# Performance work log

Hardware: AMD Instinct MI355X
Metric: run time of the kernel (lower is better)

## Reference

```python
import jax, jax.numpy as jnp
import numpy as np


def setup_inputs() -> dict:
    key = jax.random.key(0)
    k1, k2 = jax.random.split(key)
    N, K, D = 32768, 1024, 512
    x = jax.random.normal(k1, (N, D), dtype=jnp.float32)
    centers = jax.random.normal(k2, (K, D), dtype=jnp.float32)
    return {"x": x, "centers": centers}


def reference(x, centers):
    # broadcasted (x[:,None]-c[None])**2 sum without the O(N*K*D) intermediate)
    x_sq = jnp.sum(x * x, axis=-1, keepdims=True)           # [N, 1]
    c_sq = jnp.sum(centers * centers, axis=-1)              # [K]
    cross = jnp.einsum('nd,kd->nk', x, centers)             # [N, K]
    norm_squared = x_sq + c_sq[None, :] - 2.0 * cross       # [N, K]
    # exp(-d/2) / sum_k exp(-d/2) == softmax(-d/2) over clusters
    probabilities = jax.nn.softmax(-0.5 * norm_squared, axis=1)
    return probabilities
```

## Files before the change

### kernel.cpp

```cpp
#include <hip/hip_runtime.h>
#include <stdint.h>


namespace {
constexpr int N_ROWS  = 32768;
constexpr int K_CL    = 1024;
constexpr int D_DIM   = 512;
constexpr int BM      = 32;
constexpr int THREADS = 256;
constexpr int NSLICE  = 16;
}

typedef _Float16 f16_t;
typedef _Float16 f16x8 __attribute__((ext_vector_type(8)));
typedef _Float16 f16x4 __attribute__((ext_vector_type(4)));
typedef float    f32x16 __attribute__((ext_vector_type(16)));
typedef float    f32x4v __attribute__((ext_vector_type(4)));

__global__ __launch_bounds__(64) void prep_kernel(const float* __restrict__ centers,
                                                  f16_t* __restrict__ bpack,
                                                  float* __restrict__ bias) {
  const int col = blockIdx.x, lane = threadIdx.x;
  const int t  = lane >> 2;
  const int ks = (lane >> 1) & 1;
  const int kh = lane & 1;
  const float* src = centers + (size_t)col * D_DIM + lane * 8;
  f16x8 hi;
  float ssq = 0.f;
  #pragma unroll
  for (int i = 0; i < 8; ++i) {
    float v = src[i];
    ssq += v * v;
    hi[i] = (f16_t)v;
  }
  const int jh = col >> 9, cb = (col & 511) >> 5, c32 = col & 31;
  const size_t off = ((size_t)ks * 16 + cb) * 512 + (c32 * 2 + kh) * 8;
  *(f16x8*)(bpack + (size_t)(2 * t + jh) * 16384 + off) = hi;
  for (int o = 32; o; o >>= 1) ssq += __shfl_down(ssq, o, 64);
  if (lane == 0) bias[col] = -0.5f * ssq;
}

__global__ __launch_bounds__(THREADS, 2) void cluster_kernel(
    const float* __restrict__ x, const f16_t* __restrict__ bpack,
    const float* __restrict__ bias, float* __restrict__ out) {
  __shared__ __align__(16) char Ax[32768];
  __shared__ float red[4 * BM];
  __shared__ float fin[BM];

  const int tid  = threadIdx.x;
  const int w    = tid >> 6;
  const int lane = tid & 63;
  const int l31  = lane & 31;
  const int h    = lane >> 5;
  const int brow = blockIdx.x * BM;

  const char* bbase = (const char*)bpack + (w >> 1) * 32768 + (w & 1) * 8192 +
                      (l31 * 2 + h) * 16;

#define LOADB(T, KS, DST)                                                      \
  {                                                                            \
    const char* p_ = bbase + (size_t)(T) * 65536 + (KS) * 16384;               \
    _Pragma("unroll")                                                          \
    for (int cb_ = 0; cb_ < 8; ++cb_)                                          \
      (DST)[cb_] = *(const f16x8*)(p_ + cb_ * 1024);                           \
  }

  f16x8 b0[8], b1[8];
  LOADB(0, 0, b0)

  {
    const float* xsrc = x + (size_t)brow * D_DIM;
    #pragma unroll
    for (int it = 0; it < 16; ++it) {
      const int idx = it * 256 + tid;
      const int r = idx >> 7, f = idx & 127;
      f32x4v v = __builtin_nontemporal_load(
          (const f32x4v*)(xsrc + (size_t)r * D_DIM + f * 4));
      f16x4 h4;
      h4[0] = (f16_t)v[0]; h4[1] = (f16_t)v[1];
      h4[2] = (f16_t)v[2]; h4[3] = (f16_t)v[3];
      *(f16x4*)(Ax + r * 1024 + ((f * 8) ^ ((r & 7) << 4))) = h4;
    }
  }
  __syncthreads();

  f32x16 acc[8];
  #pragma unroll
  for (int cb = 0; cb < 8; ++cb)
    #pragma unroll
    for (int e = 0; e < 16; ++e) acc[cb][e] = 0.f;

  const char* abase = Ax + l31 * 1024;
  const int swz = (l31 & 7) << 4;

  #pragma unroll
  for (int T = 0; T < NSLICE; ++T) {
    const f16x8 a0 = *(const f16x8*)(abase + ((T * 64 + h * 16) ^ swz));
    const f16x8 a1 = *(const f16x8*)(abase + ((T * 64 + 32 + h * 16) ^ swz));
    LOADB(T, 1, b1)
    #pragma unroll
    for (int cb = 0; cb < 8; ++cb)
      acc[cb] = __builtin_amdgcn_mfma_f32_32x32x16_f16(a0, b0[cb], acc[cb],
                                                       0, 0, 0);
    if (T < 15) { LOADB(T + 1, 0, b0) }
    #pragma unroll
    for (int cb = 0; cb < 8; ++cb)
      acc[cb] = __builtin_amdgcn_mfma_f32_32x32x16_f16(a1, b1[cb], acc[cb],
                                                       0, 0, 0);
  }

  float bcol[8];
  #pragma unroll
  for (int cb = 0; cb < 8; ++cb)
    bcol[cb] = bias[w * 256 + cb * 32 + l31];

  float rr[16];
  #pragma unroll
  for (int reg = 0; reg < 16; ++reg) {
    float m = -3.0e38f;
    #pragma unroll
    for (int cb = 0; cb < 8; ++cb) {
      float v = acc[cb][reg] + bcol[cb];
      acc[cb][reg] = v;
      m = fmaxf(m, v);
    }
    m = fmaxf(m, __shfl_xor(m, 1, 64));
    m = fmaxf(m, __shfl_xor(m, 2, 64));
    m = fmaxf(m, __shfl_xor(m, 4, 64));
    m = fmaxf(m, __shfl_xor(m, 8, 64));
    m = fmaxf(m, __shfl_xor(m, 16, 64));
    rr[reg] = m;
  }
  if (l31 == 0) {
    #pragma unroll
    for (int reg = 0; reg < 16; ++reg)
      red[w * BM + (reg & 3) + 8 * (reg >> 2) + 4 * h] = rr[reg];
  }
  __syncthreads();
  if (tid < BM) {
    float m = red[tid];
    #pragma unroll
    for (int ww = 1; ww < 4; ++ww) m = fmaxf(m, red[ww * BM + tid]);
    fin[tid] = m;
  }
  __syncthreads();

  #pragma unroll
  for (int reg = 0; reg < 16; ++reg) {
    const float m = fin[(reg & 3) + 8 * (reg >> 2) + 4 * h];
    float s = 0.f;
    #pragma unroll
    for (int cb = 0; cb < 8; ++cb) {
      float e = __expf(acc[cb][reg] - m);
      acc[cb][reg] = e;
      s += e;
    }
    s += __shfl_xor(s, 1, 64);
    s += __shfl_xor(s, 2, 64);
    s += __shfl_xor(s, 4, 64);
    s += __shfl_xor(s, 8, 64);
    s += __shfl_xor(s, 16, 64);
    rr[reg] = s;
  }
  __syncthreads();
  if (l31 == 0) {
    #pragma unroll
    for (int reg = 0; reg < 16; ++reg)
      red[w * BM + (reg & 3) + 8 * (reg >> 2) + 4 * h] = rr[reg];
  }
  __syncthreads();
  if (tid < BM) {
    float s = 0.f;
    #pragma unroll
    for (int ww = 0; ww < 4; ++ww) s += red[ww * BM + tid];
    fin[tid] = 1.0f / s;
  }
  __syncthreads();

  #pragma unroll
  for (int reg = 0; reg < 16; ++reg) {
    const int row = (reg & 3) + 8 * (reg >> 2) + 4 * h;
    const float rs = fin[row];
    #pragma unroll
    for (int cb = 0; cb < 8; ++cb) {
      const int col = w * 256 + cb * 32 + l31;
      __builtin_nontemporal_store(acc[cb][reg] * rs,
                                  &out[(size_t)(brow + row) * K_CL + col]);
    }
  }
}

extern "C" void kernel_launch(void* const* d_in, const int* in_sizes, int n_in,
                              void* d_out, int out_size, void* d_ws, size_t ws_size,
                              hipStream_t stream) {
  const float* x       = (const float*)d_in[0];
  const float* centers = (const float*)d_in[1];
  float* out = (float*)d_out;

  f16_t* bpack = (f16_t*)d_ws;
  float* bias  = (float*)((char*)d_ws + (size_t)32 * 32768);

  prep_kernel<<<K_CL, 64, 0, stream>>>(centers, bpack, bias);
  cluster_kernel<<<N_ROWS / BM, THREADS, 0, stream>>>(x, bpack, bias, out);
}
```

Measured before the change: 92.59 us.

## Use 64-row blocks with 16 waves each computing 64x64 tiles

Each block now handles 64 rows with 1024 threads. Each of the 16 waves computes a 2x2 grid of 32x32 MFMA tiles covering 64 rows by 64 cluster columns, instead of 32 rows by 256 columns. The center packing layout is changed to match. This halves global reads of the packed centers per output row and gives each MFMA more operand reuse, at the cost of dropping the register double-buffered B prefetch and doubling shared-memory use per block. The reductions now write per-wave partials directly, which removes one barrier, but they must combine 16 waves instead of 4.

```diff
diff --git a/kernel.cpp b/kernel.cpp
--- a/kernel.cpp
+++ b/kernel.cpp
@@ -6,8 +6,9 @@
 constexpr int N_ROWS  = 32768;
 constexpr int K_CL    = 1024;
 constexpr int D_DIM   = 512;
-constexpr int BM      = 32;
-constexpr int THREADS = 256;
+constexpr int BM      = 64;
+constexpr int THREADS = 1024;
+constexpr int WAVES   = 16;
 constexpr int NSLICE  = 16;
 }
 
@@ -33,18 +34,17 @@
     ssq += v * v;
     hi[i] = (f16_t)v;
   }
-  const int jh = col >> 9, cb = (col & 511) >> 5, c32 = col & 31;
-  const size_t off = ((size_t)ks * 16 + cb) * 512 + (c32 * 2 + kh) * 8;
-  *(f16x8*)(bpack + (size_t)(2 * t + jh) * 16384 + off) = hi;
+  const int cb = col >> 5, c32 = col & 31;
+  *(f16x8*)(bpack + (size_t)(t * 2 + ks) * 16384 + cb * 512 + (c32 * 2 + kh) * 8) = hi;
   for (int o = 32; o; o >>= 1) ssq += __shfl_down(ssq, o, 64);
   if (lane == 0) bias[col] = -0.5f * ssq;
 }
 
-__global__ __launch_bounds__(THREADS, 2) void cluster_kernel(
+__global__ __launch_bounds__(THREADS, 4) void cluster_kernel(
     const float* __restrict__ x, const f16_t* __restrict__ bpack,
     const float* __restrict__ bias, float* __restrict__ out) {
-  __shared__ __align__(16) char Ax[32768];
-  __shared__ float red[4 * BM];
+  __shared__ __align__(16) char Ax[65536];
+  __shared__ float red[WAVES * BM];
   __shared__ float fin[BM];
 
   const int tid  = threadIdx.x;
@@ -54,25 +54,13 @@
   const int h    = lane >> 5;
   const int brow = blockIdx.x * BM;
 
-  const char* bbase = (const char*)bpack + (w >> 1) * 32768 + (w & 1) * 8192 +
-                      (l31 * 2 + h) * 16;
-
-#define LOADB(T, KS, DST)                                                      \
-  {                                                                            \
-    const char* p_ = bbase + (size_t)(T) * 65536 + (KS) * 16384;               \
-    _Pragma("unroll")                                                          \
-    for (int cb_ = 0; cb_ < 8; ++cb_)                                          \
-      (DST)[cb_] = *(const f16x8*)(p_ + cb_ * 1024);                           \
-  }
-
-  f16x8 b0[8], b1[8];
-  LOADB(0, 0, b0)
+  const char* bbase = (const char*)bpack + w * 2048 + (l31 * 2 + h) * 16;
 
   {
     const float* xsrc = x + (size_t)brow * D_DIM;
     #pragma unroll
-    for (int it = 0; it < 16; ++it) {
-      const int idx = it * 256 + tid;
+    for (int it = 0; it < 8; ++it) {
+      const int idx = it * 1024 + tid;
       const int r = idx >> 7, f = idx & 127;
       f32x4v v = __builtin_nontemporal_load(
           (const f32x4v*)(xsrc + (size_t)r * D_DIM + f * 4));
@@ -84,110 +72,108 @@
   }
   __syncthreads();
 
-  f32x16 acc[8];
+  f32x16 acc[2][2];
   #pragma unroll
-  for (int cb = 0; cb < 8; ++cb)
+  for (int rb = 0; rb < 2; ++rb)
     #pragma unroll
-    for (int e = 0; e < 16; ++e) acc[cb][e] = 0.f;
+    for (int cc = 0; cc < 2; ++cc)
+      #pragma unroll
+      for (int e = 0; e < 16; ++e) acc[rb][cc][e] = 0.f;
 
   const char* abase = Ax + l31 * 1024;
   const int swz = (l31 & 7) << 4;
 
   #pragma unroll
   for (int T = 0; T < NSLICE; ++T) {
-    const f16x8 a0 = *(const f16x8*)(abase + ((T * 64 + h * 16) ^ swz));
-    const f16x8 a1 = *(const f16x8*)(abase + ((T * 64 + 32 + h * 16) ^ swz));
-    LOADB(T, 1, b1)
-    #pragma unroll
-    for (int cb = 0; cb < 8; ++cb)
-      acc[cb] = __builtin_amdgcn_mfma_f32_32x32x16_f16(a0, b0[cb], acc[cb],
-                                                       0, 0, 0);
-    if (T < 15) { LOADB(T + 1, 0, b0) }
-    #pragma unroll
-    for (int cb = 0; cb < 8; ++cb)
-      acc[cb] = __builtin_amdgcn_mfma_f32_32x32x16_f16(a1, b1[cb], acc[cb],
-                                                       0, 0, 0);
+    const char* p0 = bbase + (size_t)T * 65536;
+    f16x8 b00 = *(const f16x8*)(p0);
+    f16x8 b01 = *(const f16x8*)(p0 + 1024);
+    f16x8 b10 = *(const f16x8*)(p0 + 32768);
+    f16x8 b11 = *(const f16x8*)(p0 + 32768 + 1024);
+    const int o0 = (T * 64 + h * 16) ^ swz;
+    const f16x8 a00 = *(const f16x8*)(abase + o0);
+    const f16x8 a01 = *(const f16x8*)(abase + (o0 ^ 32));
+    const f16x8 a10 = *(const f16x8*)(abase + 32768 + o0);
+    const f16x8 a11 = *(const f16x8*)(abase + 32768 + (o0 ^ 32));
+    acc[0][0] = __builtin_amdgcn_mfma_f32_32x32x16_f16(a00, b00, acc[0][0], 0, 0, 0);
+    acc[0][1] = __builtin_amdgcn_mfma_f32_32x32x16_f16(a00, b01, acc[0][1], 0, 0, 0);
+    acc[1][0] = __builtin_amdgcn_mfma_f32_32x32x16_f16(a10, b00, acc[1][0], 0, 0, 0);
+    acc[1][1] = __builtin_amdgcn_mfma_f32_32x32x16_f16(a10, b01, acc[1][1], 0, 0, 0);
+    acc[0][0] = __builtin_amdgcn_mfma_f32_32x32x16_f16(a01, b10, acc[0][0], 0, 0, 0);
+    acc[0][1] = __builtin_amdgcn_mfma_f32_32x32x16_f16(a01, b11, acc[0][1], 0, 0, 0);
+    acc[1][0] = __builtin_amdgcn_mfma_f32_32x32x16_f16(a11, b10, acc[1][0], 0, 0, 0);
+    acc[1][1] = __builtin_amdgcn_mfma_f32_32x32x16_f16(a11, b11, acc[1][1], 0, 0, 0);
   }
 
-  float bcol[8];
+  float bcol[2];
   #pragma unroll
-  for (int cb = 0; cb < 8; ++cb)
-    bcol[cb] = bias[w * 256 + cb * 32 + l31];
+  for (int cc = 0; cc < 2; ++cc)
+    bcol[cc] = bias[w * 64 + cc * 32 + l31];
 
-  float rr[16];
   #pragma unroll
-  for (int reg = 0; reg < 16; ++reg) {
-    float m = -3.0e38f;
+  for (int rb = 0; rb < 2; ++rb)
     #pragma unroll
-    for (int cb = 0; cb < 8; ++cb) {
-      float v = acc[cb][reg] + bcol[cb];
-      acc[cb][reg] = v;
-      m = fmaxf(m, v);
+    for (int reg = 0; reg < 16; ++reg) {
+      float v0 = acc[rb][0][reg] + bcol[0];
+      float v1 = acc[rb][1][reg] + bcol[1];
+      acc[rb][0][reg] = v0;
+      acc[rb][1][reg] = v1;
+      float m = fmaxf(v0, v1);
+      m = fmaxf(m, __shfl_xor(m, 1, 64));
+      m = fmaxf(m, __shfl_xor(m, 2, 64));
+      m = fmaxf(m, __shfl_xor(m, 4, 64));
+      m = fmaxf(m, __shfl_xor(m, 8, 64));
+      m = fmaxf(m, __shfl_xor(m, 16, 64));
+      if (l31 == 0)
+        red[w * BM + rb * 32 + (reg & 3) + 8 * (reg >> 2) + 4 * h] = m;
     }
-    m = fmaxf(m, __shfl_xor(m, 1, 64));
-    m = fmaxf(m, __shfl_xor(m, 2, 64));
-    m = fmaxf(m, __shfl_xor(m, 4, 64));
-    m = fmaxf(m, __shfl_xor(m, 8, 64));
-    m = fmaxf(m, __shfl_xor(m, 16, 64));
-    rr[reg] = m;
-  }
-  if (l31 == 0) {
-    #pragma unroll
-    for (int reg = 0; reg < 16; ++reg)
-      red[w * BM + (reg & 3) + 8 * (reg >> 2) + 4 * h] = rr[reg];
-  }
   __syncthreads();
   if (tid < BM) {
     float m = red[tid];
     #pragma unroll
-    for (int ww = 1; ww < 4; ++ww) m = fmaxf(m, red[ww * BM + tid]);
+    for (int ww = 1; ww < WAVES; ++ww) m = fmaxf(m, red[ww * BM + tid]);
     fin[tid] = m;
   }
   __syncthreads();
 
   #pragma unroll
-  for (int reg = 0; reg < 16; ++reg) {
-    const float m = fin[(reg & 3) + 8 * (reg >> 2) + 4 * h];
-    float s = 0.f;
+  for (int rb = 0; rb < 2; ++rb)
     #pragma unroll
-    for (int cb = 0; cb < 8; ++cb) {
-      float e = __expf(acc[cb][reg] - m);
-      acc[cb][reg] = e;
-      s += e;
+    for (int reg = 0; reg < 16; ++reg) {
+      const float m = fin[rb * 32 + (reg & 3) + 8 * (reg >> 2) + 4 * h];
+      float e0 = __expf(acc[rb][0][reg] - m);
+      float e1 = __expf(acc[rb][1][reg] - m);
+      acc[rb][0][reg] = e0;
+      acc[rb][1][reg] = e1;
+      float s = e0 + e1;
+      s += __shfl_xor(s, 1, 64);
+      s += __shfl_xor(s, 2, 64);
+      s += __shfl_xor(s, 4, 64);
+      s += __shfl_xor(s, 8, 64);
+      s += __shfl_xor(s, 16, 64);
+      if (l31 == 1)
+        red[w * BM + rb * 32 + (reg & 3) + 8 * (reg >> 2) + 4 * h] = s;
     }
-    s += __shfl_xor(s, 1, 64);
-    s += __shfl_xor(s, 2, 64);
-    s += __shfl_xor(s, 4, 64);
-    s += __shfl_xor(s, 8, 64);
-    s += __shfl_xor(s, 16, 64);
-    rr[reg] = s;
-  }
-  __syncthreads();
-  if (l31 == 0) {
-    #pragma unroll
-    for (int reg = 0; reg < 16; ++reg)
-      red[w * BM + (reg & 3) + 8 * (reg >> 2) + 4 * h] = rr[reg];
-  }
   __syncthreads();
   if (tid < BM) {
     float s = 0.f;
     #pragma unroll
-    for (int ww = 0; ww < 4; ++ww) s += red[ww * BM + tid];
+    for (int ww = 0; ww < WAVES; ++ww) s += red[ww * BM + tid];
     fin[tid] = 1.0f / s;
   }
   __syncthreads();
 
   #pragma unroll
-  for (int reg = 0; reg < 16; ++reg) {
-    const int row = (reg & 3) + 8 * (reg >> 2) + 4 * h;
-    const float rs = fin[row];
+  for (int rb = 0; rb < 2; ++rb)
     #pragma unroll
-    for (int cb = 0; cb < 8; ++cb) {
-      const int col = w * 256 + cb * 32 + l31;
-      __builtin_nontemporal_store(acc[cb][reg] * rs,
-                                  &out[(size_t)(brow + row) * K_CL + col]);
+    for (int reg = 0; reg < 16; ++reg) {
+      const int row = rb * 32 + (reg & 3) + 8 * (reg >> 2) + 4 * h;
+      const float rs = fin[row];
+      #pragma unroll
+      for (int cc = 0; cc < 2; ++cc)
+        __builtin_nontemporal_store(acc[rb][cc][reg] * rs,
+            &out[(size_t)(brow + row) * K_CL + w * 64 + cc * 32 + l31]);
     }
-  }
 }
 
 extern "C" void kernel_launch(void* const* d_in, const int* in_sizes, int n_in,
```

New measurement: 99.38 us. +7.3%, slower.
